# Kernel optimization log

Measured on AMD Instinct MI355X. Metric: run time of the kernel, lower is better.

Reference implementation:

```python
import jax, jax.numpy as jnp
import numpy as np

B_J0 = 0.01   # baseline threshold
DT = 1.0
BETA = 1.8    # adaptation strength
LENS = 0.5
SCALE = 6.0
HIGHT = 0.15
GAMMA = 0.5


def _gauss(x, mu, sigma):
    return jnp.exp(-(x - mu) ** 2 / (2.0 * sigma ** 2)) / jnp.sqrt(2.0 * jnp.pi) / sigma


@jax.custom_vjp
def spike_fn(x):
    return (x > 0).astype(x.dtype)


def _spike_fwd(x):
    return spike_fn(x), x


def _spike_bwd(x, g):
    # multi-gaussian surrogate gradient (config.gradient_type == 'MG')
    temp = (_gauss(x, 0.0, LENS) * (1.0 + HIGHT)
            - _gauss(x, LENS, SCALE * LENS) * HIGHT
            - _gauss(x, -LENS, SCALE * LENS) * HIGHT)
    return (g * temp * GAMMA,)


spike_fn.defvjp(_spike_fwd, _spike_bwd)


def setup_inputs() -> dict:
    key = jax.random.key(0)
    ks = jax.random.split(key, 20)
    Bt, T, I, H, O = 256, 250, 700, 128, 20
    f32 = jnp.float32
    return {
        'x': jax.random.uniform(ks[0], (Bt, T, I), dtype=f32),
        'mask': jnp.ones((2, H, H), dtype=f32),
        'w_ih1': (jax.random.normal(ks[1], (I, H), dtype=f32) / np.sqrt(I).astype(np.float32)),
        'b_ih1': jnp.zeros((H,), f32),
        'w_h1h1': (jax.random.normal(ks[2], (H, H), dtype=f32) / np.sqrt(H).astype(np.float32)),
        'b_h1h1': jnp.zeros((H,), f32),
        'w_h1h2': (jax.random.normal(ks[3], (H, H), dtype=f32) / np.sqrt(H).astype(np.float32)),
        'b_h1h2': jnp.zeros((H,), f32),
        'w_h2h2': (jax.random.normal(ks[4], (H, H), dtype=f32) / np.sqrt(H).astype(np.float32)),
        'b_h2h2': jnp.zeros((H,), f32),
        'w_h2o': (jax.random.normal(ks[5], (H, O), dtype=f32) / np.sqrt(H).astype(np.float32)),
        'b_h2o': jnp.zeros((O,), f32),
        'tau_adp_h1': 150.0 + 10.0 * jax.random.normal(ks[6], (H,), dtype=f32),
        'tau_adp_h2': 150.0 + 10.0 * jax.random.normal(ks[7], (H,), dtype=f32),
        'tau_m_h1': 20.0 + 5.0 * jax.random.normal(ks[8], (H,), dtype=f32),
        'tau_m_h2': 20.0 + 5.0 * jax.random.normal(ks[9], (H,), dtype=f32),
        'tau_m_o': 20.0 + 5.0 * jax.random.normal(ks[10], (O,), dtype=f32),
        'hid1_mem0': jax.random.uniform(ks[11], (Bt, H), dtype=f32),
        'hid2_mem0': jax.random.uniform(ks[12], (Bt, H), dtype=f32),
        'out_mem0': jax.random.uniform(ks[13], (Bt, O), dtype=f32),
    }


def _forward(x, mask, w_ih1, b_ih1, w_h1h1, b_h1h1, w_h1h2, b_h1h2,
             w_h2h2, b_h2h2, w_h2o, b_h2o, tau_adp_h1, tau_adp_h2,
             tau_m_h1, tau_m_h2, tau_m_o, hid1_mem0, hid2_mem0, out_mem0):
    Bt, T, _ = x.shape
    H = w_ih1.shape[1]
    O = w_h2o.shape[1]
    # dropout mask applied to recurrent weights (weights stored [in, out])
    w11 = w_h1h1 * mask[0]
    w22 = w_h2h2 * mask[1]
    a1 = jnp.exp(-DT / tau_m_h1)
    r1 = jnp.exp(-DT / tau_adp_h1)
    a2 = jnp.exp(-DT / tau_m_h2)
    r2 = jnp.exp(-DT / tau_adp_h2)
    ao = jnp.exp(-DT / tau_m_o)
    # precompute input projection for all timesteps: [T, B, H]
    xin = jnp.einsum('bti,ih->tbh', x, w_ih1) + b_ih1

    def step(carry, inps):
        h1m, h1s, h2m, h2s, om, b1, b2, acc, s1, s2 = carry
        xt, t = inps
        # layer 1 (adaptive LIF)
        i1 = xt + h1s @ w11 + b_h1h1
        b1 = r1 * b1 + (1.0 - r1) * h1s
        B1 = B_J0 + BETA * b1
        h1m = h1m * a1 + (1.0 - a1) * i1 - B1 * h1s * DT
        h1s = spike_fn(h1m - B1)
        s1 = s1 + h1s
        # layer 2 (adaptive LIF)
        i2 = h1s @ w_h1h2 + b_h1h2 + h2s @ w22 + b_h2h2
        b2 = r2 * b2 + (1.0 - r2) * h2s
        B2 = B_J0 + BETA * b2
        h2m = h2m * a2 + (1.0 - a2) * i2 - B2 * h2s * DT
        h2s = spike_fn(h2m - B2)
        s2 = s2 + h2s
        # leaky-integrator readout (no spike)
        io = h2s @ w_h2o + b_h2o
        om = om * ao + (1.0 - ao) * io
        acc = acc + jnp.where(t > 10, jax.nn.softmax(om, axis=-1), 0.0)
        return (h1m, h1s, h2m, h2s, om, b1, b2, acc, s1, s2), None

    zH = jnp.zeros((Bt, H), x.dtype)
    carry0 = (hid1_mem0, zH, hid2_mem0, zH, out_mem0,
              jnp.full((Bt, H), B_J0, x.dtype), jnp.full((Bt, H), B_J0, x.dtype),
              jnp.zeros((Bt, O), x.dtype), zH, zH)
    carry, _ = jax.lax.scan(step, carry0, (xin, jnp.arange(T)))
    output, s1, s2 = carry[7], carry[8], carry[9]
    A_norm = jnp.sum(jnp.abs(w11)) + jnp.sum(jnp.abs(w22))
    return output, s1 / T, s2 / T, A_norm


def reference(x, mask, w_ih1, b_ih1, w_h1h1, b_h1h1, w_h1h2, b_h1h2,
              w_h2h2, b_h2h2, w_h2o, b_h2o, tau_adp_h1, tau_adp_h2,
              tau_m_h1, tau_m_h2, tau_m_o, hid1_mem0, hid2_mem0, out_mem0):
    return _forward(x, mask, w_ih1, b_ih1, w_h1h1, b_h1h1, w_h1h2, b_h1h2,
                    w_h2h2, b_h2h2, w_h2o, b_h2o, tau_adp_h1, tau_adp_h2,
                    tau_m_h1, tau_m_h2, tau_m_o, hid1_mem0, hid2_mem0, out_mem0)
```

## Files before the change

kernel.cpp:

```cpp
#include <hip/hip_runtime.h>
#include <math.h>

#define TT 250
#define BT 256
#define HN 128
#define ON 20
#define KIN 700
#define NKT 22

#define XIN_OFF 0
#define WPKH_OFF 8192000
#define WPKL_OFF 8237056

typedef __attribute__((ext_vector_type(8))) short bf16x8;
typedef __attribute__((ext_vector_type(4))) float f32x4;

__device__ __forceinline__ unsigned short bf16rne(float f) {
    unsigned u = __float_as_uint(f);
    unsigned r = u + 0x7fffu + ((u >> 16) & 1u);
    return (unsigned short)(r >> 16);
}
__device__ __forceinline__ void hilo(float v, short& h, short& l) {
    unsigned short hh = bf16rne(v);
    float vh = __uint_as_float((unsigned)hh << 16);
    h = (short)hh;
    l = (short)bf16rne(v - vh);
}

__global__ __launch_bounds__(256) void packw(const float* __restrict__ w,
                                             unsigned short* __restrict__ ph,
                                             unsigned short* __restrict__ pl) {
    int i = blockIdx.x * 256 + threadIdx.x;
    int k = i >> 7, c = i & 127;
    float v = (k < KIN) ? w[k * HN + c] : 0.f;
    short h, l;
    hilo(v, h, l);
    int dst = (((k >> 5) * 8 + (c >> 4)) * 64 + (((k >> 3) & 3) * 16 + (c & 15))) * 8 + (k & 7);
    ph[dst] = (unsigned short)h;
    pl[dst] = (unsigned short)l;
}

__global__ __launch_bounds__(256) void gemm_in(const float* __restrict__ x,
        const bf16x8* __restrict__ wph, const bf16x8* __restrict__ wpl,
        const float* __restrict__ bias1, const float* __restrict__ bias2,
        float* __restrict__ xin) {
    const int tid = threadIdx.x;
    const int w = tid >> 6, lane = tid & 63;
    const int q = lane >> 4, li = lane & 15;
    const long mrow = (long)blockIdx.x * 64 + w * 16 + li;
    const float* xr = x + mrow * KIN + q * 8;

    float b12[8];
#pragma unroll
    for (int nt = 0; nt < 8; nt++) {
        int col = nt * 16 + li;
        b12[nt] = bias1[col] + bias2[col];
    }

    f32x4 acc[8];
#pragma unroll
    for (int nt = 0; nt < 8; nt++) acc[nt] = (f32x4){0.f, 0.f, 0.f, 0.f};

    for (int kt = 0; kt < NKT; kt++) {
        float av[8];
        const float* p = xr + kt * 32;
        *(float4*)&av[0] = *(const float4*)p;
        if (kt == NKT - 1 && q == 3) {
            av[4] = 0.f; av[5] = 0.f; av[6] = 0.f; av[7] = 0.f;
        } else {
            *(float4*)&av[4] = *(const float4*)(p + 4);
        }
        bf16x8 ah, al;
#pragma unroll
        for (int j = 0; j < 8; j++) {
            short h, l;
            hilo(av[j], h, l);
            ah[j] = h; al[j] = l;
        }
#pragma unroll
        for (int nt = 0; nt < 8; nt++) {
            bf16x8 bh = wph[(kt * 8 + nt) * 64 + lane];
            bf16x8 bl = wpl[(kt * 8 + nt) * 64 + lane];
            acc[nt] = __builtin_amdgcn_mfma_f32_16x16x32_bf16(ah, bh, acc[nt], 0, 0, 0);
            acc[nt] = __builtin_amdgcn_mfma_f32_16x16x32_bf16(al, bh, acc[nt], 0, 0, 0);
            acc[nt] = __builtin_amdgcn_mfma_f32_16x16x32_bf16(ah, bl, acc[nt], 0, 0, 0);
        }
    }

#pragma unroll
    for (int r = 0; r < 4; r++) {
        int m = blockIdx.x * 64 + w * 16 + q * 4 + r;
        int bq = (int)(((unsigned long long)m * 67109ull) >> 24);
        int tt = m - bq * 250;
        float* dst = xin + ((size_t)tt * BT + bq) * HN;
#pragma unroll
        for (int nt = 0; nt < 8; nt++) dst[nt * 16 + li] = acc[nt][r] + b12[nt];
    }
}

__global__ __launch_bounds__(512, 2) void snn_scan(
    const float* __restrict__ xin, const float* __restrict__ mask,
    const float* __restrict__ w_h1h1, const float* __restrict__ w_h1h2,
    const float* __restrict__ b_h1h2, const float* __restrict__ w_h2h2,
    const float* __restrict__ b_h2h2, const float* __restrict__ w_h2o,
    const float* __restrict__ b_h2o, const float* __restrict__ tau_adp1,
    const float* __restrict__ tau_adp2, const float* __restrict__ taum1,
    const float* __restrict__ taum2, const float* __restrict__ taumo,
    const float* __restrict__ h1m0, const float* __restrict__ h2m0,
    const float* __restrict__ om0, float* __restrict__ out) {

    __shared__ __align__(16) unsigned short sA1[2 * 2048];
    __shared__ __align__(16) unsigned short sA2[2048];
    __shared__ float omb[16 * ON];
    __shared__ float red[8];

    const int tid = threadIdx.x;
    const int w = tid >> 6, lane = tid & 63;
    const int q = lane >> 4, li = lane & 15;
    const int col = w * 16 + li;
    const int r0 = blockIdx.x * 16;

    bf16x8 h11[4], l11[4], h22[4], l22[4], h12[4], l12[4], hO[4], lO[4];
    const int ocol = (w == 6) ? li : 16 + li;
    const bool oval = (w >= 6) && (ocol < ON);
    float pn = 0.f;
#pragma unroll
    for (int kt = 0; kt < 4; kt++) {
#pragma unroll
        for (int j = 0; j < 8; j++) {
            const int k = kt * 32 + q * 8 + j;
            const int idx = k * HN + col;
            float v11 = w_h1h1[idx] * mask[idx];
            float v22 = w_h2h2[idx] * mask[HN * HN + idx];
            float v12 = w_h1h2[idx];
            pn += fabsf(v11) + fabsf(v22);
            short hh, ll;
            hilo(v11, hh, ll); h11[kt][j] = hh; l11[kt][j] = ll;
            hilo(v22, hh, ll); h22[kt][j] = hh; l22[kt][j] = ll;
            hilo(v12, hh, ll); h12[kt][j] = hh; l12[kt][j] = ll;
            float vO = oval ? w_h2o[k * ON + ocol] : 0.f;
            hilo(vO, hh, ll); hO[kt][j] = hh; lO[kt][j] = ll;
        }
    }

    const float a1 = expf(-1.f / taum1[col]);
    const float r1 = expf(-1.f / tau_adp1[col]);
    const float a2 = expf(-1.f / taum2[col]);
    const float r2 = expf(-1.f / tau_adp2[col]);
    const float cc2 = b_h1h2[col] + b_h2h2[col];
    float h1m[4], h2m[4], b1[4], b2[4], c1[4], c2n[4];
    unsigned s1bits = 0, s2bits = 0;
#pragma unroll
    for (int r = 0; r < 4; r++) {
        h1m[r] = h1m0[(r0 + q * 4 + r) * HN + col];
        h2m[r] = h2m0[(r0 + q * 4 + r) * HN + col];
        b1[r] = 0.01f; b2[r] = 0.01f; c1[r] = 0.f; c2n[r] = 0.f;
    }
    const float ao = oval ? expf(-1.f / taumo[ocol]) : 0.f;
    const float bo = oval ? b_h2o[ocol] : 0.f;
    float om[4];
#pragma unroll
    for (int r = 0; r < 4; r++)
        om[r] = oval ? om0[(r0 + q * 4 + r) * ON + ocol] : 0.f;
    const int sm = lane >> 2, ob = (lane & 3) * 5;
    float accs[5] = {0.f, 0.f, 0.f, 0.f, 0.f};

    {
        unsigned* z1 = (unsigned*)sA1;
        unsigned* z2 = (unsigned*)sA2;
        z1[tid] = 0u; z1[tid + 512] = 0u;
        z2[tid] = 0u; z2[tid + 512] = 0u;
    }

#pragma unroll
    for (int off = 32; off > 0; off >>= 1) pn += __shfl_down(pn, off);
    if (lane == 0) red[w] = pn;
    __syncthreads();
    if (tid == 0 && blockIdx.x == 0) {
        float s = 0.f;
#pragma unroll
        for (int i = 0; i < 8; i++) s += red[i];
        out[70656] = s;
    }

    const int wbase = (w >> 1) * 512 + (((2 * w + (li >> 3)) & 3) * 16 + q * 4) * 8 + (li & 7);

    const bf16x8* sa1v = (const bf16x8*)sA1;
    const bf16x8* sa2v = (const bf16x8*)sA2;
    const unsigned short ONE = 0x3F80u;

    for (int t = 0; t < TT; t++) {
        const int rb = (t & 1) * 256;
        const int wb = ((t + 1) & 1) * 2048;

        float xt[4];
#pragma unroll
        for (int r = 0; r < 4; r++)
            xt[r] = xin[((size_t)t * BT + r0 + q * 4 + r) * HN + col];

        bf16x8 f1[4], f2[4];
#pragma unroll
        for (int kt = 0; kt < 4; kt++) {
            f1[kt] = sa1v[rb + kt * 64 + lane];
            f2[kt] = sa2v[kt * 64 + lane];
        }
        f32x4 aI = {0.f, 0.f, 0.f, 0.f}, aG = {0.f, 0.f, 0.f, 0.f};
#pragma unroll
        for (int kt = 0; kt < 4; kt++) {
            aI = __builtin_amdgcn_mfma_f32_16x16x32_bf16(f1[kt], h11[kt], aI, 0, 0, 0);
            aI = __builtin_amdgcn_mfma_f32_16x16x32_bf16(f1[kt], l11[kt], aI, 0, 0, 0);
            aG = __builtin_amdgcn_mfma_f32_16x16x32_bf16(f2[kt], h22[kt], aG, 0, 0, 0);
            aG = __builtin_amdgcn_mfma_f32_16x16x32_bf16(f2[kt], l22[kt], aG, 0, 0, 0);
        }
        if (w >= 6) {
            f32x4 aO = {0.f, 0.f, 0.f, 0.f};
#pragma unroll
            for (int kt = 0; kt < 4; kt++) {
                aO = __builtin_amdgcn_mfma_f32_16x16x32_bf16(f2[kt], hO[kt], aO, 0, 0, 0);
                aO = __builtin_amdgcn_mfma_f32_16x16x32_bf16(f2[kt], lO[kt], aO, 0, 0, 0);
            }
            if (t >= 1) {
#pragma unroll
                for (int r = 0; r < 4; r++) {
                    om[r] = ao * om[r] + (1.f - ao) * (bo + aO[r]);
                    if (oval) omb[(q * 4 + r) * ON + ocol] = om[r];
                }
            }
        }
#pragma unroll
        for (int r = 0; r < 4; r++) {
            const float sv = (float)((s1bits >> r) & 1u);
            const float i1 = xt[r] + aI[r];
            b1[r] = r1 * b1[r] + (1.f - r1) * sv;
            const float B = 0.01f + 1.8f * b1[r];
            h1m[r] = a1 * h1m[r] + (1.f - a1) * i1 - B * sv;
            const bool sp = (h1m[r] - B) > 0.f;
            s1bits = sp ? (s1bits | (1u << r)) : (s1bits & ~(1u << r));
            c1[r] += sp ? 1.f : 0.f;
            sA1[wb + wbase + r * 8] = sp ? ONE : (unsigned short)0;
        }
        __syncthreads();

        bf16x8 g1[4];
#pragma unroll
        for (int kt = 0; kt < 4; kt++) g1[kt] = sa1v[(wb >> 3) + kt * 64 + lane];
        f32x4 aJ = {0.f, 0.f, 0.f, 0.f};
#pragma unroll
        for (int kt = 0; kt < 4; kt++) {
            aJ = __builtin_amdgcn_mfma_f32_16x16x32_bf16(g1[kt], h12[kt], aJ, 0, 0, 0);
            aJ = __builtin_amdgcn_mfma_f32_16x16x32_bf16(g1[kt], l12[kt], aJ, 0, 0, 0);
        }
        if (w == 7 && t >= 12) {
            float v[5], e[5];
            float mx = -1e30f;
#pragma unroll
            for (int i = 0; i < 5; i++) { v[i] = omb[sm * ON + ob + i]; mx = fmaxf(mx, v[i]); }
            mx = fmaxf(mx, __shfl_xor(mx, 1));
            mx = fmaxf(mx, __shfl_xor(mx, 2));
            float se = 0.f;
#pragma unroll
            for (int i = 0; i < 5; i++) { e[i] = __expf(v[i] - mx); se += e[i]; }
            se += __shfl_xor(se, 1);
            se += __shfl_xor(se, 2);
            const float inv = 1.f / se;
#pragma unroll
            for (int i = 0; i < 5; i++) accs[i] += e[i] * inv;
        }
#pragma unroll
        for (int r = 0; r < 4; r++) {
            const float sv = (float)((s2bits >> r) & 1u);
            const float i2 = aJ[r] + aG[r] + cc2;
            b2[r] = r2 * b2[r] + (1.f - r2) * sv;
            const float B = 0.01f + 1.8f * b2[r];
            h2m[r] = a2 * h2m[r] + (1.f - a2) * i2 - B * sv;
            const bool sp = (h2m[r] - B) > 0.f;
            s2bits = sp ? (s2bits | (1u << r)) : (s2bits & ~(1u << r));
            c2n[r] += sp ? 1.f : 0.f;
            sA2[wbase + r * 8] = sp ? ONE : (unsigned short)0;
        }
        __syncthreads();
    }

    if (w >= 6) {
        bf16x8 f2[4];
#pragma unroll
        for (int kt = 0; kt < 4; kt++) f2[kt] = sa2v[kt * 64 + lane];
        f32x4 aO = {0.f, 0.f, 0.f, 0.f};
#pragma unroll
        for (int kt = 0; kt < 4; kt++) {
            aO = __builtin_amdgcn_mfma_f32_16x16x32_bf16(f2[kt], hO[kt], aO, 0, 0, 0);
            aO = __builtin_amdgcn_mfma_f32_16x16x32_bf16(f2[kt], lO[kt], aO, 0, 0, 0);
        }
#pragma unroll
        for (int r = 0; r < 4; r++) {
            om[r] = ao * om[r] + (1.f - ao) * (bo + aO[r]);
            if (oval) omb[(q * 4 + r) * ON + ocol] = om[r];
        }
    }
    __syncthreads();
    if (w == 7) {
        float v[5], e[5];
        float mx = -1e30f;
#pragma unroll
        for (int i = 0; i < 5; i++) { v[i] = omb[sm * ON + ob + i]; mx = fmaxf(mx, v[i]); }
        mx = fmaxf(mx, __shfl_xor(mx, 1));
        mx = fmaxf(mx, __shfl_xor(mx, 2));
        float se = 0.f;
#pragma unroll
        for (int i = 0; i < 5; i++) { e[i] = __expf(v[i] - mx); se += e[i]; }
        se += __shfl_xor(se, 1);
        se += __shfl_xor(se, 2);
        const float inv = 1.f / se;
#pragma unroll
        for (int i = 0; i < 5; i++) out[(r0 + sm) * ON + ob + i] = accs[i] + e[i] * inv;
    }
#pragma unroll
    for (int r = 0; r < 4; r++) {
        out[5120 + (r0 + q * 4 + r) * HN + col] = c1[r] * (1.f / 250.f);
        out[37888 + (r0 + q * 4 + r) * HN + col] = c2n[r] * (1.f / 250.f);
    }
}

extern "C" void kernel_launch(void* const* d_in, const int* in_sizes, int n_in,
                              void* d_out, int out_size, void* d_ws, size_t ws_size,
                              hipStream_t stream) {
    const float* x        = (const float*)d_in[0];
    const float* mask     = (const float*)d_in[1];
    const float* w_ih1    = (const float*)d_in[2];
    const float* b_ih1    = (const float*)d_in[3];
    const float* w_h1h1   = (const float*)d_in[4];
    const float* b_h1h1   = (const float*)d_in[5];
    const float* w_h1h2   = (const float*)d_in[6];
    const float* b_h1h2   = (const float*)d_in[7];
    const float* w_h2h2   = (const float*)d_in[8];
    const float* b_h2h2   = (const float*)d_in[9];
    const float* w_h2o    = (const float*)d_in[10];
    const float* b_h2o    = (const float*)d_in[11];
    const float* tau_adp1 = (const float*)d_in[12];
    const float* tau_adp2 = (const float*)d_in[13];
    const float* taum1    = (const float*)d_in[14];
    const float* taum2    = (const float*)d_in[15];
    const float* taumo    = (const float*)d_in[16];
    const float* h1m0     = (const float*)d_in[17];
    const float* h2m0     = (const float*)d_in[18];
    const float* om0      = (const float*)d_in[19];
    float* out = (float*)d_out;
    float* ws  = (float*)d_ws;

    float* xin = ws + XIN_OFF;
    unsigned short* wph = (unsigned short*)(ws + WPKH_OFF);
    unsigned short* wpl = (unsigned short*)(ws + WPKL_OFF);

    packw<<<352, 256, 0, stream>>>(w_ih1, wph, wpl);
    gemm_in<<<1000, 256, 0, stream>>>(x, (const bf16x8*)wph, (const bf16x8*)wpl,
                                      b_ih1, b_h1h1, xin);
    snn_scan<<<16, 512, 0, stream>>>(xin, mask, w_h1h1, w_h1h2, b_h1h2, w_h2h2,
                                     b_h2h2, w_h2o, b_h2o, tau_adp1, tau_adp2,
                                     taum1, taum2, taumo, h1m0, h2m0, om0, out);
}
```

Before: 655.7 us.

## Double-buffer weight tiles in LDS for input GEMM and prefetch in scan loop

```diff
diff --git a/kernel.cpp b/kernel.cpp
--- a/kernel.cpp
+++ b/kernel.cpp
@@ -25,6 +25,16 @@
     float vh = __uint_as_float((unsigned)hh << 16);
     h = (short)hh;
     l = (short)bf16rne(v - vh);
+}
+
+#define LBAR() do { asm volatile("s_waitcnt lgkmcnt(0)" ::: "memory"); \
+                    __builtin_amdgcn_s_barrier();                      \
+                    asm volatile("" ::: "memory"); } while (0)
+
+__device__ __forceinline__ void gl_lds16(const void* g, void* l) {
+    __builtin_amdgcn_global_load_lds(
+        (const __attribute__((address_space(1))) unsigned int*)g,
+        (__attribute__((address_space(3))) unsigned int*)l, 16, 0, 0);
 }
 
 __global__ __launch_bounds__(256) void packw(const float* __restrict__ w,
@@ -40,36 +50,56 @@
     pl[dst] = (unsigned short)l;
 }
 
-__global__ __launch_bounds__(256) void gemm_in(const float* __restrict__ x,
-        const bf16x8* __restrict__ wph, const bf16x8* __restrict__ wpl,
+__device__ __forceinline__ void stage_kt(const unsigned short* __restrict__ wph,
+                                         const unsigned short* __restrict__ wpl,
+                                         void* buf, int kt, int tid) {
+    const char* sh = (const char*)wph + kt * 8192 + tid * 16;
+    const char* sl = (const char*)wpl + kt * 8192 + tid * 16;
+    char* b = (char*)buf;
+    const int wb = (tid >> 6) * 1024;
+    gl_lds16(sh,        b + wb);
+    gl_lds16(sh + 4096, b + wb + 4096);
+    gl_lds16(sl,        b + wb + 8192);
+    gl_lds16(sl + 4096, b + wb + 12288);
+}
+
+__device__ __forceinline__ void loadx8(float* av, const float* p, bool tailq3) {
+    *(float4*)&av[0] = *(const float4*)p;
+    if (tailq3) {
+        av[4] = 0.f; av[5] = 0.f; av[6] = 0.f; av[7] = 0.f;
+    } else {
+        *(float4*)&av[4] = *(const float4*)(p + 4);
+    }
+}
+
+__global__ __launch_bounds__(256, 4) void gemm_in(const float* __restrict__ x,
+        const unsigned short* __restrict__ wph, const unsigned short* __restrict__ wpl,
         const float* __restrict__ bias1, const float* __restrict__ bias2,
         float* __restrict__ xin) {
+    __shared__ __align__(16) unsigned char wbuf[2][16384];
     const int tid = threadIdx.x;
     const int w = tid >> 6, lane = tid & 63;
     const int q = lane >> 4, li = lane & 15;
     const long mrow = (long)blockIdx.x * 64 + w * 16 + li;
     const float* xr = x + mrow * KIN + q * 8;
 
-    float b12[8];
-#pragma unroll
-    for (int nt = 0; nt < 8; nt++) {
-        int col = nt * 16 + li;
-        b12[nt] = bias1[col] + bias2[col];
-    }
-
     f32x4 acc[8];
 #pragma unroll
     for (int nt = 0; nt < 8; nt++) acc[nt] = (f32x4){0.f, 0.f, 0.f, 0.f};
 
+    stage_kt(wph, wpl, wbuf[0], 0, tid);
+    float av[8];
+    loadx8(av, xr, false);
+    __syncthreads();
+
+#pragma unroll 2
     for (int kt = 0; kt < NKT; kt++) {
-        float av[8];
-        const float* p = xr + kt * 32;
-        *(float4*)&av[0] = *(const float4*)p;
-        if (kt == NKT - 1 && q == 3) {
-            av[4] = 0.f; av[5] = 0.f; av[6] = 0.f; av[7] = 0.f;
-        } else {
-            *(float4*)&av[4] = *(const float4*)(p + 4);
-        }
+        if (kt + 1 < NKT)
+            stage_kt(wph, wpl, wbuf[(kt + 1) & 1], kt + 1, tid);
+        float avn[8];
+        if (kt + 1 < NKT)
+            loadx8(avn, xr + (kt + 1) * 32, (kt + 1 == NKT - 1) && (q == 3));
+
         bf16x8 ah, al;
 #pragma unroll
         for (int j = 0; j < 8; j++) {
@@ -77,16 +107,30 @@
             hilo(av[j], h, l);
             ah[j] = h; al[j] = l;
         }
-#pragma unroll
+
+        const bf16x8* cv = (const bf16x8*)&wbuf[kt & 1][0];
+#pragma unroll 2
         for (int nt = 0; nt < 8; nt++) {
-            bf16x8 bh = wph[(kt * 8 + nt) * 64 + lane];
-            bf16x8 bl = wpl[(kt * 8 + nt) * 64 + lane];
+            bf16x8 bh = cv[nt * 64 + lane];
+            bf16x8 bl = cv[512 + nt * 64 + lane];
             acc[nt] = __builtin_amdgcn_mfma_f32_16x16x32_bf16(ah, bh, acc[nt], 0, 0, 0);
             acc[nt] = __builtin_amdgcn_mfma_f32_16x16x32_bf16(al, bh, acc[nt], 0, 0, 0);
             acc[nt] = __builtin_amdgcn_mfma_f32_16x16x32_bf16(ah, bl, acc[nt], 0, 0, 0);
         }
-    }
-
+
+        if (kt + 1 < NKT) {
+#pragma unroll
+            for (int j = 0; j < 8; j++) av[j] = avn[j];
+        }
+        __syncthreads();
+    }
+
+    float b12[8];
+#pragma unroll
+    for (int nt = 0; nt < 8; nt++) {
+        int c = nt * 16 + li;
+        b12[nt] = bias1[c] + bias2[c];
+    }
 #pragma unroll
     for (int r = 0; r < 4; r++) {
         int m = blockIdx.x * 64 + w * 16 + q * 4 + r;
@@ -98,7 +142,7 @@
     }
 }
 
-__global__ __launch_bounds__(512, 2) void snn_scan(
+__global__ __launch_bounds__(512, 1) void snn_scan(
     const float* __restrict__ xin, const float* __restrict__ mask,
     const float* __restrict__ w_h1h1, const float* __restrict__ w_h1h2,
     const float* __restrict__ b_h1h2, const float* __restrict__ w_h2h2,
@@ -189,26 +233,32 @@
     const bf16x8* sa2v = (const bf16x8*)sA2;
     const unsigned short ONE = 0x3F80u;
 
+    bf16x8 f1c[4];
+    const bf16x8 zf = {0, 0, 0, 0, 0, 0, 0, 0};
+#pragma unroll
+    for (int kt = 0; kt < 4; kt++) f1c[kt] = zf;
+
+    float xt[4], xtn[4];
+#pragma unroll
+    for (int r = 0; r < 4; r++)
+        xt[r] = xin[((size_t)0 * BT + r0 + q * 4 + r) * HN + col];
+
     for (int t = 0; t < TT; t++) {
-        const int rb = (t & 1) * 256;
         const int wb = ((t + 1) & 1) * 2048;
 
-        float xt[4];
+        const int tn = (t + 1 < TT) ? t + 1 : t;
 #pragma unroll
         for (int r = 0; r < 4; r++)
-            xt[r] = xin[((size_t)t * BT + r0 + q * 4 + r) * HN + col];
-
-        bf16x8 f1[4], f2[4];
+            xtn[r] = xin[((size_t)tn * BT + r0 + q * 4 + r) * HN + col];
+
+        bf16x8 f2[4];
+#pragma unroll
+        for (int kt = 0; kt < 4; kt++) f2[kt] = sa2v[kt * 64 + lane];
+        f32x4 aI = {0.f, 0.f, 0.f, 0.f}, aG = {0.f, 0.f, 0.f, 0.f};
 #pragma unroll
         for (int kt = 0; kt < 4; kt++) {
-            f1[kt] = sa1v[rb + kt * 64 + lane];
-            f2[kt] = sa2v[kt * 64 + lane];
-        }
-        f32x4 aI = {0.f, 0.f, 0.f, 0.f}, aG = {0.f, 0.f, 0.f, 0.f};
-#pragma unroll
-        for (int kt = 0; kt < 4; kt++) {
-            aI = __builtin_amdgcn_mfma_f32_16x16x32_bf16(f1[kt], h11[kt], aI, 0, 0, 0);
-            aI = __builtin_amdgcn_mfma_f32_16x16x32_bf16(f1[kt], l11[kt], aI, 0, 0, 0);
+            aI = __builtin_amdgcn_mfma_f32_16x16x32_bf16(f1c[kt], h11[kt], aI, 0, 0, 0);
+            aI = __builtin_amdgcn_mfma_f32_16x16x32_bf16(f1c[kt], l11[kt], aI, 0, 0, 0);
             aG = __builtin_amdgcn_mfma_f32_16x16x32_bf16(f2[kt], h22[kt], aG, 0, 0, 0);
             aG = __builtin_amdgcn_mfma_f32_16x16x32_bf16(f2[kt], l22[kt], aG, 0, 0, 0);
         }
@@ -239,7 +289,7 @@
             c1[r] += sp ? 1.f : 0.f;
             sA1[wb + wbase + r * 8] = sp ? ONE : (unsigned short)0;
         }
-        __syncthreads();
+        LBAR();
 
         bf16x8 g1[4];
 #pragma unroll
@@ -278,7 +328,11 @@
             c2n[r] += sp ? 1.f : 0.f;
             sA2[wbase + r * 8] = sp ? ONE : (unsigned short)0;
         }
-        __syncthreads();
+#pragma unroll
+        for (int kt = 0; kt < 4; kt++) f1c[kt] = g1[kt];
+#pragma unroll
+        for (int r = 0; r < 4; r++) xt[r] = xtn[r];
+        LBAR();
     }
 
     if (w >= 6) {
@@ -352,8 +406,7 @@
     unsigned short* wpl = (unsigned short*)(ws + WPKL_OFF);
 
     packw<<<352, 256, 0, stream>>>(w_ih1, wph, wpl);
-    gemm_in<<<1000, 256, 0, stream>>>(x, (const bf16x8*)wph, (const bf16x8*)wpl,
-                                      b_ih1, b_h1h1, xin);
+    gemm_in<<<1000, 256, 0, stream>>>(x, wph, wpl, b_ih1, b_h1h1, xin);
     snn_scan<<<16, 512, 0, stream>>>(xin, mask, w_h1h1, w_h1h2, b_h1h2, w_h2h2,
                                      b_h2h2, w_h2o, b_h2o, tau_adp1, tau_adp2,
                                      taum1, taum2, taumo, h1m0, h2m0, om0, out);
```

After: 636.4 us. -2.9%, faster.
